# Kernel optimization log

Measured on AMD Instinct MI355X. Metric: run time of the kernel, lower is better.

The kernel has to match this reference:

```python
import jax, jax.numpy as jnp
import numpy as np

D_MODEL = 1024
N_HEADS = 16
HEAD_DIM = 64
T = 4096
ROT = HEAD_DIM // 2          # 32 channels get rotary
PAIR = ROT // 2              # 16 cos/sin frequencies
EPS = 1e-6
SCALE = 0.12                 # constant attention scale (not 1/sqrt(d))
ROPE_BASE = 10000.0
VOCAB = 50257


def setup_inputs() -> dict:
    key = jax.random.key(0)
    k_x, k_qkv, k_o, k_tok = jax.random.split(key, 4)
    bound = 0.5 / np.sqrt(D_MODEL)
    x = jax.random.normal(k_x, (1, T, D_MODEL), dtype=jnp.float32)
    w_qkv = jax.random.uniform(k_qkv, (3 * D_MODEL, D_MODEL), jnp.float32, -bound, bound)
    # module uses zero_init for w_o; use small random so output is non-trivial
    w_o = jax.random.uniform(k_o, (D_MODEL, D_MODEL), jnp.float32, -bound, bound)
    q_norm_w = jnp.ones((HEAD_DIM,), jnp.float32)
    k_norm_w = jnp.ones((HEAD_DIM,), jnp.float32)
    tokens = jax.random.randint(k_tok, (1, T), 0, VOCAB, dtype=jnp.int64)
    pos = jnp.arange(T, dtype=jnp.int64)
    # RotaryCache: inv_freq over pair dims, cos/sin of t * inv_freq
    inv_freq = 1.0 / (ROPE_BASE ** (jnp.arange(PAIR, dtype=jnp.float32) / PAIR))
    freqs = jnp.arange(T, dtype=jnp.float32)[:, None] * inv_freq[None, :]  # [T, PAIR]
    return {
        "x": x, "tokens": tokens, "pos": pos,
        "w_qkv": w_qkv, "w_o": w_o,
        "q_norm_w": q_norm_w, "k_norm_w": k_norm_w,
        "cos": jnp.cos(freqs), "sin": jnp.sin(freqs),
        "window_tokens": 1024, "block_size": 128,
    }


def _rmsnorm(x, w):
    var = jnp.mean(x * x, axis=-1, keepdims=True)
    return x * jax.lax.rsqrt(var + EPS) * w


def reference(x, tokens, pos, w_qkv, w_o, q_norm_w, k_norm_w, cos, sin,
              window_tokens, block_size):
    B, Tq, C = x.shape
    H, Dh = N_HEADS, HEAD_DIM
    qkv = x @ w_qkv.T                                  # [B, T, 3C]
    q, k, v = jnp.split(qkv, 3, axis=-1)

    def to_bhtd(t):
        return t.reshape(B, Tq, H, Dh).transpose(0, 2, 1, 3)
    q, k, v = to_bhtd(q), to_bhtd(k), to_bhtd(v)

    q = _rmsnorm(q, q_norm_w)
    k = _rmsnorm(k, k_norm_w)

    # half-truncated RoPE: rotate first ROT channels pairwise (even/odd)
    c = cos[pos][None, None]                           # [1,1,T,PAIR]
    s = sin[pos][None, None]

    def rope_rotate(t):
        t1, t2 = t[..., :ROT], t[..., ROT:]
        even, odd = t1[..., 0::2], t1[..., 1::2]
        r_even = even * c - odd * s
        r_odd = even * s + odd * c
        t1r = jnp.stack([r_even, r_odd], axis=-1).reshape(t1.shape)
        return jnp.concatenate([t1r, t2], axis=-1)

    q = rope_rotate(q)
    k = rope_rotate(k)

    v = v * 0.5                                        # no value-embed branch

    scores = jnp.einsum('bhtd,bhsd->bhts', q, k) * SCALE
    idx = jnp.arange(Tq)
    diff = idx[:, None] - idx[None, :]
    allowed = (diff >= 0) & (diff < window_tokens)     # sliding causal window
    scores = jnp.where(allowed, scores, -jnp.inf)
    p = jax.nn.softmax(scores, axis=-1)
    out = jnp.einsum('bhts,bhsd->bhtd', p, v)
    out = out.transpose(0, 2, 1, 3).reshape(B, Tq, C)
    return out @ w_o.T
```

## Files before the change

### kernel.cpp

```cpp
#include <hip/hip_runtime.h>


typedef __bf16 bf16x8 __attribute__((ext_vector_type(8)));
typedef __bf16 bf16x2 __attribute__((ext_vector_type(2)));
typedef float f32x4 __attribute__((ext_vector_type(4)));
typedef unsigned short u16x8 __attribute__((ext_vector_type(8)));
typedef unsigned short u16x4 __attribute__((ext_vector_type(4)));

#define MFMA16(a, b, c) __builtin_amdgcn_mfma_f32_16x16x32_bf16((a), (b), (c), 0, 0, 0)

__device__ __forceinline__ unsigned short f2bf(float f) {
    unsigned int u = __float_as_uint(f);
    u += 0x7fffu + ((u >> 16) & 1u);
    return (unsigned short)(u >> 16);
}
__device__ __forceinline__ float bf2f(unsigned short h) {
    return __uint_as_float(((unsigned int)h) << 16);
}
__device__ __forceinline__ unsigned int pk2bf(float a, float b) {
#if __has_builtin(__builtin_amdgcn_cvt_pk_bf16_f32)
    bf16x2 v = __builtin_amdgcn_cvt_pk_bf16_f32(a, b);
    return __builtin_bit_cast(unsigned int, v);
#else
    return (unsigned int)f2bf(a) | ((unsigned int)f2bf(b) << 16);
#endif
}

__device__ __forceinline__ void gl_lds16(const void* g, void* l) {
    typedef __attribute__((address_space(1))) unsigned int GU;
    typedef __attribute__((address_space(3))) unsigned int LU;
    __builtin_amdgcn_global_load_lds((GU*)(unsigned long long)g,
                                     (LU*)(unsigned int)(unsigned long long)l,
                                     16, 0, 0);
}

__global__ void cvt_bf16_kernel(const float* __restrict__ src,
                                unsigned short* __restrict__ dst, int n4) {
    int i = blockIdx.x * blockDim.x + threadIdx.x;
    if (i >= n4) return;
    float4 f = ((const float4*)src)[i];
    u16x4 o;
    o[0] = f2bf(f.x); o[1] = f2bf(f.y); o[2] = f2bf(f.z); o[3] = f2bf(f.w);
    ((u16x4*)dst)[i] = o;
}

template <int BM, bool F32OUT>
__global__ __launch_bounds__(256) void gemm_bt(
    const unsigned short* __restrict__ A,
    const unsigned short* __restrict__ Bt,
    void* __restrict__ Cp, int N, int K) {
    __shared__ unsigned short As[BM * 32];
    __shared__ unsigned short Bs[128 * 32];
    constexpr int MT = BM / 32;
    const int tid = threadIdx.x;
    const int wave = tid >> 6, lane = tid & 63;
    const int quad = lane >> 4, l16 = lane & 15;
    const int m0 = blockIdx.x * BM, n0 = blockIdx.y * 128;
    const int wm = (wave >> 1) * (BM / 2), wn = (wave & 1) * 64;

    f32x4 acc[MT][4];
#pragma unroll
    for (int i = 0; i < MT; ++i)
#pragma unroll
        for (int j = 0; j < 4; ++j) acc[i][j] = (f32x4){0.f, 0.f, 0.f, 0.f};

    for (int k0 = 0; k0 < K; k0 += 32) {
#pragma unroll
        for (int i = 0; i < BM / 64; ++i) {
            const int c = wave * (BM / 64) + i;
            const int e = (c * 64 + lane) * 8;
            const int r = e >> 5, col = e & 31;
            gl_lds16(A + (size_t)(m0 + r) * K + (k0 + col), &As[c * 512]);
        }
#pragma unroll
        for (int i = 0; i < 2; ++i) {
            const int c = wave * 2 + i;
            const int e = (c * 64 + lane) * 8;
            const int r = e >> 5, col = e & 31;
            gl_lds16(Bt + (size_t)(n0 + r) * K + (k0 + col), &Bs[c * 512]);
        }
        __syncthreads();
        bf16x8 af[MT], bfr[4];
#pragma unroll
        for (int mt = 0; mt < MT; ++mt)
            af[mt] = *(const bf16x8*)&As[(wm + mt * 16 + l16) * 32 + quad * 8];
#pragma unroll
        for (int nt = 0; nt < 4; ++nt)
            bfr[nt] = *(const bf16x8*)&Bs[(wn + nt * 16 + l16) * 32 + quad * 8];
#pragma unroll
        for (int mt = 0; mt < MT; ++mt)
#pragma unroll
            for (int nt = 0; nt < 4; ++nt)
                acc[mt][nt] = MFMA16(af[mt], bfr[nt], acc[mt][nt]);
        __syncthreads();
    }
#pragma unroll
    for (int mt = 0; mt < MT; ++mt)
#pragma unroll
        for (int nt = 0; nt < 4; ++nt)
#pragma unroll
            for (int r = 0; r < 4; ++r) {
                const int row = m0 + wm + mt * 16 + quad * 4 + r;
                const int col = n0 + wn + nt * 16 + l16;
                const float v = acc[mt][nt][r];
                if (F32OUT)
                    ((float*)Cp)[(size_t)row * N + col] = v;
                else
                    ((unsigned short*)Cp)[(size_t)row * N + col] = f2bf(v);
            }
}

__global__ __launch_bounds__(256) void rope_pack_kernel(
    const unsigned short* __restrict__ qkv,
    const float* __restrict__ cosb, const float* __restrict__ sinb,
    const float* __restrict__ qw, const float* __restrict__ kw,
    unsigned short* __restrict__ Qb,
    unsigned short* __restrict__ Kb,
    unsigned short* __restrict__ Vt)
{
    __shared__ unsigned short vlds[64][65];
    const int h = blockIdx.y;
    const int t0 = blockIdx.x * 64;
    const int tid = threadIdx.x;
    const int tl = tid >> 2, dq = tid & 3;
    const int t = t0 + tl;
    const unsigned short* base = qkv + (size_t)t * 3072 + h * 64 + dq * 16;

    float q[16], k[16], v[16];
    {
        u16x8 a0 = *(const u16x8*)(base);
        u16x8 a1 = *(const u16x8*)(base + 8);
        u16x8 b0 = *(const u16x8*)(base + 1024);
        u16x8 b1 = *(const u16x8*)(base + 1032);
        u16x8 c0 = *(const u16x8*)(base + 2048);
        u16x8 c1 = *(const u16x8*)(base + 2056);
#pragma unroll
        for (int i = 0; i < 8; ++i) {
            q[i] = bf2f(a0[i]); q[8 + i] = bf2f(a1[i]);
            k[i] = bf2f(b0[i]); k[8 + i] = bf2f(b1[i]);
            v[i] = bf2f(c0[i]); v[8 + i] = bf2f(c1[i]);
        }
    }
    float sq = 0.f, sk = 0.f;
#pragma unroll
    for (int i = 0; i < 16; ++i) { sq += q[i] * q[i]; sk += k[i] * k[i]; }
    sq += __shfl_xor(sq, 1); sq += __shfl_xor(sq, 2);
    sk += __shfl_xor(sk, 1); sk += __shfl_xor(sk, 2);
    const float rq = rsqrtf(sq * (1.f / 64.f) + 1e-6f);
    const float rk = rsqrtf(sk * (1.f / 64.f) + 1e-6f);
#pragma unroll
    for (int i = 0; i < 16; ++i) {
        q[i] *= rq * qw[dq * 16 + i];
        k[i] *= rk * kw[dq * 16 + i];
    }
    if (dq < 2) {
#pragma unroll
        for (int p = 0; p < 8; ++p) {
            const int gp = dq * 8 + p;
            const float c = cosb[t * 16 + gp], s = sinb[t * 16 + gp];
            float e = q[2 * p], o = q[2 * p + 1];
            q[2 * p] = e * c - o * s; q[2 * p + 1] = e * s + o * c;
            e = k[2 * p]; o = k[2 * p + 1];
            k[2 * p] = e * c - o * s; k[2 * p + 1] = e * s + o * c;
        }
    }
    const size_t oo = ((size_t)h * 4096 + t) * 64 + dq * 16;
    u16x8 w0, w1;
#pragma unroll
    for (int i = 0; i < 8; ++i) { w0[i] = f2bf(q[i]); w1[i] = f2bf(q[8 + i]); }
    *(u16x8*)(Qb + oo) = w0; *(u16x8*)(Qb + oo + 8) = w1;
#pragma unroll
    for (int i = 0; i < 8; ++i) { w0[i] = f2bf(k[i]); w1[i] = f2bf(k[8 + i]); }
    *(u16x8*)(Kb + oo) = w0; *(u16x8*)(Kb + oo + 8) = w1;

#pragma unroll
    for (int i = 0; i < 16; ++i) vlds[tl][dq * 16 + i] = f2bf(v[i] * 0.5f);
    __syncthreads();
#pragma unroll
    for (int i = 0; i < 8; ++i) { w0[i] = vlds[dq * 16 + i][tl]; w1[i] = vlds[dq * 16 + 8 + i][tl]; }
    const size_t vo = ((size_t)h * 64 + tl) * 4096 + t0 + dq * 16;
    *(u16x8*)(Vt + vo) = w0; *(u16x8*)(Vt + vo + 8) = w1;
}

#define PSTR 72

template <int MODE>
__device__ __forceinline__ void attn_step(
    int s0, int tq, int wave, int quad, int l16, int krow, int kcol,
    const unsigned short* __restrict__ Kh, const unsigned short* __restrict__ Vh,
    unsigned short* Ks0, unsigned short* Ks1,
    unsigned short* Vs0, unsigned short* Vs1, unsigned short* Pw,
    const bf16x8 qf0, const bf16x8 qf1, f32x4 (&o)[4], float& lsum)
{
    __syncthreads();
    const unsigned short* kb = Kh + (size_t)(s0 + krow) * 64 + kcol;
    const unsigned short* vb = Vh + (size_t)krow * 4096 + s0 + kcol;
    gl_lds16(kb,      &Ks0[wave * 512]);
    gl_lds16(kb + 32, &Ks1[wave * 512]);
    gl_lds16(vb,      &Vs0[wave * 512]);
    gl_lds16(vb + 32, &Vs1[wave * 512]);
    __syncthreads();

    const float c = 0.17312340490667046f;
#pragma unroll
    for (int i = 0; i < 4; ++i) {
        const bf16x8 kf0 = *(const bf16x8*)&Ks0[(i * 16 + l16) * 32 + quad * 8];
        const bf16x8 kf1 = *(const bf16x8*)&Ks1[(i * 16 + l16) * 32 + quad * 8];
        f32x4 z = (f32x4){0.f, 0.f, 0.f, 0.f};
        z = MFMA16(kf0, qf0, z);
        z = MFMA16(kf1, qf1, z);
        float p[4];
#pragma unroll
        for (int r = 0; r < 4; ++r) {
            float e = exp2f(z[r] * c);
            if (MODE == 1) {
                const int s = s0 + i * 16 + quad * 4 + r;
                e = ((tq - s) < 1024) ? e : 0.f;
            }
            if (MODE == 2) {
                const int s = s0 + i * 16 + quad * 4 + r;
                e = (s <= tq) ? e : 0.f;
            }
            p[r] = e;
            lsum += e;
        }
        uint2 pk;
        pk.x = pk2bf(p[0], p[1]);
        pk.y = pk2bf(p[2], p[3]);
        *(uint2*)&Pw[l16 * PSTR + i * 16 + quad * 4] = pk;
    }
    const bf16x8 pf0 = *(const bf16x8*)&Pw[l16 * PSTR + quad * 8];
    const bf16x8 pf1 = *(const bf16x8*)&Pw[l16 * PSTR + 32 + quad * 8];
#pragma unroll
    for (int dt = 0; dt < 4; ++dt) {
        const bf16x8 vf0 = *(const bf16x8*)&Vs0[(dt * 16 + l16) * 32 + quad * 8];
        const bf16x8 vf1 = *(const bf16x8*)&Vs1[(dt * 16 + l16) * 32 + quad * 8];
        o[dt] = MFMA16(pf0, vf0, o[dt]);
        o[dt] = MFMA16(pf1, vf1, o[dt]);
    }
}

__global__ __launch_bounds__(256) void attn_kernel(
    const unsigned short* __restrict__ Qb,
    const unsigned short* __restrict__ Kb,
    const unsigned short* __restrict__ Vt,
    unsigned short* __restrict__ att)
{
    __shared__ unsigned short Ks0[64 * 32];
    __shared__ unsigned short Ks1[64 * 32];
    __shared__ unsigned short Vs0[64 * 32];
    __shared__ unsigned short Vs1[64 * 32];
    __shared__ unsigned short P[4][16 * PSTR];

    const int h = blockIdx.y;
    const int t0 = blockIdx.x * 64;
    const int tid = threadIdx.x;
    const int wave = tid >> 6, lane = tid & 63;
    const int quad = lane >> 4, l16 = lane & 15;
    const int qt0 = t0 + wave * 16;
    const int tq = qt0 + l16;
    const int krow = tid >> 2, kcol = (tid & 3) * 8;

    const unsigned short* Qh = Qb + (size_t)h * 4096 * 64;
    const unsigned short* Kh = Kb + (size_t)h * 4096 * 64;
    const unsigned short* Vh = Vt + (size_t)h * 64 * 4096;

    const bf16x8 qf0 = *(const bf16x8*)&Qh[(qt0 + l16) * 64 + quad * 8];
    const bf16x8 qf1 = *(const bf16x8*)&Qh[(qt0 + l16) * 64 + 32 + quad * 8];

    f32x4 o[4];
#pragma unroll
    for (int dt = 0; dt < 4; ++dt) o[dt] = (f32x4){0.f, 0.f, 0.f, 0.f};
    float lsum = 0.f;
    unsigned short* Pw = P[wave];

    int s0 = (t0 >= 1024) ? (t0 - 1024) : 0;
    if (t0 >= 1024) {
        attn_step<1>(s0, tq, wave, quad, l16, krow, kcol, Kh, Vh,
                     Ks0, Ks1, Vs0, Vs1, Pw, qf0, qf1, o, lsum);
        s0 += 64;
    }
    for (; s0 < t0; s0 += 64)
        attn_step<0>(s0, tq, wave, quad, l16, krow, kcol, Kh, Vh,
                     Ks0, Ks1, Vs0, Vs1, Pw, qf0, qf1, o, lsum);
    attn_step<2>(t0, tq, wave, quad, l16, krow, kcol, Kh, Vh,
                 Ks0, Ks1, Vs0, Vs1, Pw, qf0, qf1, o, lsum);

    lsum += __shfl_xor(lsum, 16);
    lsum += __shfl_xor(lsum, 32);
    float lr[4];
#pragma unroll
    for (int r = 0; r < 4; ++r) lr[r] = 1.f / __shfl(lsum, quad * 4 + r);
#pragma unroll
    for (int dt = 0; dt < 4; ++dt)
#pragma unroll
        for (int r = 0; r < 4; ++r)
            att[(size_t)(qt0 + quad * 4 + r) * 1024 + h * 64 + dt * 16 + l16] =
                f2bf(o[dt][r] * lr[r]);
}

extern "C" void kernel_launch(void* const* d_in, const int* in_sizes, int n_in,
                              void* d_out, int out_size, void* d_ws, size_t ws_size,
                              hipStream_t stream) {
    const float* x    = (const float*)d_in[0];
    const float* wqkv = (const float*)d_in[3];
    const float* wo   = (const float*)d_in[4];
    const float* qw   = (const float*)d_in[5];
    const float* kw   = (const float*)d_in[6];
    const float* cosb = (const float*)d_in[7];
    const float* sinb = (const float*)d_in[8];

    char* ws = (char*)d_ws;
    if (ws_size < (size_t)72 * 1024 * 1024) return;
    unsigned short* xb    = (unsigned short*)(ws + ((size_t)0 << 20));
    unsigned short* wqkvb = (unsigned short*)(ws + ((size_t)8 << 20));
    unsigned short* wob   = (unsigned short*)(ws + ((size_t)14 << 20));
    unsigned short* qkvb  = (unsigned short*)(ws + ((size_t)16 << 20));
    unsigned short* Qb    = (unsigned short*)(ws + ((size_t)40 << 20));
    unsigned short* Kb    = (unsigned short*)(ws + ((size_t)48 << 20));
    unsigned short* Vt    = (unsigned short*)(ws + ((size_t)56 << 20));
    unsigned short* attb  = (unsigned short*)(ws + ((size_t)64 << 20));

    cvt_bf16_kernel<<<4096, 256, 0, stream>>>(x, xb, 4096 * 1024 / 4);
    cvt_bf16_kernel<<<3072, 256, 0, stream>>>(wqkv, wqkvb, 3072 * 1024 / 4);
    cvt_bf16_kernel<<<1024, 256, 0, stream>>>(wo, wob, 1024 * 1024 / 4);

    gemm_bt<128, false><<<dim3(32, 24), 256, 0, stream>>>(xb, wqkvb, qkvb, 3072, 1024);

    rope_pack_kernel<<<dim3(64, 16), 256, 0, stream>>>(qkvb, cosb, sinb, qw, kw, Qb, Kb, Vt);

    attn_kernel<<<dim3(64, 16), 256, 0, stream>>>(Qb, Kb, Vt, attb);

    gemm_bt<64, true><<<dim3(64, 8), 256, 0, stream>>>(attb, wob, (float*)d_out, 1024, 1024);
}
```

Before: 213.9 us.

## Fuse RMSNorm/RoPE/V-transpose into QKV GEMM epilogue and merge conversion kernels

The QKV GEMM epilogue now applies per-head RMSNorm, half RoPE and the V scale-and-transpose straight from the accumulators. This removes the separate rope_pack kernel and the bf16 qkv intermediate round-trip through memory. The three fp32-to-bf16 conversions are merged into one launch. The attention grid is flattened and remapped so adjacent blocks cover different heads. The epilogue writes scalar bf16 values with strided stores, which may coalesce worse than before.

```diff
diff --git a/kernel.cpp b/kernel.cpp
--- a/kernel.cpp
+++ b/kernel.cpp
@@ -34,152 +34,131 @@
                                      16, 0, 0);
 }
 
-__global__ void cvt_bf16_kernel(const float* __restrict__ src,
-                                unsigned short* __restrict__ dst, int n4) {
-    int i = blockIdx.x * blockDim.x + threadIdx.x;
-    if (i >= n4) return;
-    float4 f = ((const float4*)src)[i];
+__global__ void cvt3_kernel(const float* __restrict__ x,
+                            const float* __restrict__ wqkv,
+                            const float* __restrict__ wo,
+                            unsigned short* __restrict__ xb,
+                            unsigned short* __restrict__ wqkvb,
+                            unsigned short* __restrict__ wob) {
+    int i = blockIdx.x * 256 + threadIdx.x;
+    const float* src;
+    unsigned short* dst;
+    int off;
+    if (i < 1048576) { src = x; dst = xb; off = i; }
+    else if (i < 1835008) { src = wqkv; dst = wqkvb; off = i - 1048576; }
+    else { src = wo; dst = wob; off = i - 1835008; }
+    float4 f = ((const float4*)src)[off];
     u16x4 o;
     o[0] = f2bf(f.x); o[1] = f2bf(f.y); o[2] = f2bf(f.z); o[3] = f2bf(f.w);
-    ((u16x4*)dst)[i] = o;
-}
-
-template <int BM, bool F32OUT>
-__global__ __launch_bounds__(256) void gemm_bt(
+    ((u16x4*)dst)[off] = o;
+}
+
+__global__ __launch_bounds__(256) void gemm_qkv(
     const unsigned short* __restrict__ A,
     const unsigned short* __restrict__ Bt,
-    void* __restrict__ Cp, int N, int K) {
-    __shared__ unsigned short As[BM * 32];
-    __shared__ unsigned short Bs[128 * 32];
-    constexpr int MT = BM / 32;
-    const int tid = threadIdx.x;
-    const int wave = tid >> 6, lane = tid & 63;
-    const int quad = lane >> 4, l16 = lane & 15;
-    const int m0 = blockIdx.x * BM, n0 = blockIdx.y * 128;
-    const int wm = (wave >> 1) * (BM / 2), wn = (wave & 1) * 64;
-
-    f32x4 acc[MT][4];
-#pragma unroll
-    for (int i = 0; i < MT; ++i)
-#pragma unroll
-        for (int j = 0; j < 4; ++j) acc[i][j] = (f32x4){0.f, 0.f, 0.f, 0.f};
-
-    for (int k0 = 0; k0 < K; k0 += 32) {
-#pragma unroll
-        for (int i = 0; i < BM / 64; ++i) {
-            const int c = wave * (BM / 64) + i;
-            const int e = (c * 64 + lane) * 8;
-            const int r = e >> 5, col = e & 31;
-            gl_lds16(A + (size_t)(m0 + r) * K + (k0 + col), &As[c * 512]);
-        }
-#pragma unroll
-        for (int i = 0; i < 2; ++i) {
-            const int c = wave * 2 + i;
-            const int e = (c * 64 + lane) * 8;
-            const int r = e >> 5, col = e & 31;
-            gl_lds16(Bt + (size_t)(n0 + r) * K + (k0 + col), &Bs[c * 512]);
-        }
-        __syncthreads();
-        bf16x8 af[MT], bfr[4];
-#pragma unroll
-        for (int mt = 0; mt < MT; ++mt)
-            af[mt] = *(const bf16x8*)&As[(wm + mt * 16 + l16) * 32 + quad * 8];
-#pragma unroll
-        for (int nt = 0; nt < 4; ++nt)
-            bfr[nt] = *(const bf16x8*)&Bs[(wn + nt * 16 + l16) * 32 + quad * 8];
-#pragma unroll
-        for (int mt = 0; mt < MT; ++mt)
-#pragma unroll
-            for (int nt = 0; nt < 4; ++nt)
-                acc[mt][nt] = MFMA16(af[mt], bfr[nt], acc[mt][nt]);
-        __syncthreads();
-    }
-#pragma unroll
-    for (int mt = 0; mt < MT; ++mt)
-#pragma unroll
-        for (int nt = 0; nt < 4; ++nt)
-#pragma unroll
-            for (int r = 0; r < 4; ++r) {
-                const int row = m0 + wm + mt * 16 + quad * 4 + r;
-                const int col = n0 + wn + nt * 16 + l16;
-                const float v = acc[mt][nt][r];
-                if (F32OUT)
-                    ((float*)Cp)[(size_t)row * N + col] = v;
-                else
-                    ((unsigned short*)Cp)[(size_t)row * N + col] = f2bf(v);
-            }
-}
-
-__global__ __launch_bounds__(256) void rope_pack_kernel(
-    const unsigned short* __restrict__ qkv,
     const float* __restrict__ cosb, const float* __restrict__ sinb,
     const float* __restrict__ qw, const float* __restrict__ kw,
     unsigned short* __restrict__ Qb,
     unsigned short* __restrict__ Kb,
     unsigned short* __restrict__ Vt)
 {
-    __shared__ unsigned short vlds[64][65];
-    const int h = blockIdx.y;
-    const int t0 = blockIdx.x * 64;
+    __shared__ unsigned short As[128 * 32];
+    __shared__ unsigned short Bs[128 * 32];
+    __shared__ unsigned short tb[4][64 * 16];
     const int tid = threadIdx.x;
-    const int tl = tid >> 2, dq = tid & 3;
-    const int t = t0 + tl;
-    const unsigned short* base = qkv + (size_t)t * 3072 + h * 64 + dq * 16;
-
-    float q[16], k[16], v[16];
-    {
-        u16x8 a0 = *(const u16x8*)(base);
-        u16x8 a1 = *(const u16x8*)(base + 8);
-        u16x8 b0 = *(const u16x8*)(base + 1024);
-        u16x8 b1 = *(const u16x8*)(base + 1032);
-        u16x8 c0 = *(const u16x8*)(base + 2048);
-        u16x8 c1 = *(const u16x8*)(base + 2056);
-#pragma unroll
-        for (int i = 0; i < 8; ++i) {
-            q[i] = bf2f(a0[i]); q[8 + i] = bf2f(a1[i]);
-            k[i] = bf2f(b0[i]); k[8 + i] = bf2f(b1[i]);
-            v[i] = bf2f(c0[i]); v[8 + i] = bf2f(c1[i]);
-        }
-    }
-    float sq = 0.f, sk = 0.f;
-#pragma unroll
-    for (int i = 0; i < 16; ++i) { sq += q[i] * q[i]; sk += k[i] * k[i]; }
-    sq += __shfl_xor(sq, 1); sq += __shfl_xor(sq, 2);
-    sk += __shfl_xor(sk, 1); sk += __shfl_xor(sk, 2);
-    const float rq = rsqrtf(sq * (1.f / 64.f) + 1e-6f);
-    const float rk = rsqrtf(sk * (1.f / 64.f) + 1e-6f);
-#pragma unroll
-    for (int i = 0; i < 16; ++i) {
-        q[i] *= rq * qw[dq * 16 + i];
-        k[i] *= rk * kw[dq * 16 + i];
-    }
-    if (dq < 2) {
-#pragma unroll
-        for (int p = 0; p < 8; ++p) {
-            const int gp = dq * 8 + p;
-            const float c = cosb[t * 16 + gp], s = sinb[t * 16 + gp];
-            float e = q[2 * p], o = q[2 * p + 1];
-            q[2 * p] = e * c - o * s; q[2 * p + 1] = e * s + o * c;
-            e = k[2 * p]; o = k[2 * p + 1];
-            k[2 * p] = e * c - o * s; k[2 * p + 1] = e * s + o * c;
-        }
-    }
-    const size_t oo = ((size_t)h * 4096 + t) * 64 + dq * 16;
-    u16x8 w0, w1;
-#pragma unroll
-    for (int i = 0; i < 8; ++i) { w0[i] = f2bf(q[i]); w1[i] = f2bf(q[8 + i]); }
-    *(u16x8*)(Qb + oo) = w0; *(u16x8*)(Qb + oo + 8) = w1;
-#pragma unroll
-    for (int i = 0; i < 8; ++i) { w0[i] = f2bf(k[i]); w1[i] = f2bf(k[8 + i]); }
-    *(u16x8*)(Kb + oo) = w0; *(u16x8*)(Kb + oo + 8) = w1;
-
-#pragma unroll
-    for (int i = 0; i < 16; ++i) vlds[tl][dq * 16 + i] = f2bf(v[i] * 0.5f);
-    __syncthreads();
-#pragma unroll
-    for (int i = 0; i < 8; ++i) { w0[i] = vlds[dq * 16 + i][tl]; w1[i] = vlds[dq * 16 + 8 + i][tl]; }
-    const size_t vo = ((size_t)h * 64 + tl) * 4096 + t0 + dq * 16;
-    *(u16x8*)(Vt + vo) = w0; *(u16x8*)(Vt + vo + 8) = w1;
+    const int wave = tid >> 6, lane = tid & 63;
+    const int quad = lane >> 4, l16 = lane & 15;
+    const int m0 = blockIdx.x * 128, n0 = blockIdx.y * 128;
+    const int wm = (wave >> 1) * 64, wn = (wave & 1) * 64;
+    (void)wn;
+
+    f32x4 acc[4][4];
+#pragma unroll
+    for (int i = 0; i < 4; ++i)
+#pragma unroll
+        for (int j = 0; j < 4; ++j) acc[i][j] = (f32x4){0.f, 0.f, 0.f, 0.f};
+
+    for (int k0 = 0; k0 < 1024; k0 += 32) {
+#pragma unroll
+        for (int i = 0; i < 2; ++i) {
+            const int c = wave * 2 + i;
+            const int e = (c * 64 + lane) * 8;
+            const int r = e >> 5, col = e & 31;
+            gl_lds16(A + (size_t)(m0 + r) * 1024 + (k0 + col), &As[c * 512]);
+            gl_lds16(Bt + (size_t)(n0 + r) * 1024 + (k0 + col), &Bs[c * 512]);
+        }
+        __syncthreads();
+        bf16x8 af[4], bfr[4];
+#pragma unroll
+        for (int mt = 0; mt < 4; ++mt)
+            af[mt] = *(const bf16x8*)&As[(wm + mt * 16 + l16) * 32 + quad * 8];
+#pragma unroll
+        for (int nt = 0; nt < 4; ++nt)
+            bfr[nt] = *(const bf16x8*)&Bs[((wave & 1) * 64 + nt * 16 + l16) * 32 + quad * 8];
+#pragma unroll
+        for (int mt = 0; mt < 4; ++mt)
+#pragma unroll
+            for (int nt = 0; nt < 4; ++nt)
+                acc[mt][nt] = MFMA16(af[mt], bfr[nt], acc[mt][nt]);
+        __syncthreads();
+    }
+
+    const int region = blockIdx.y >> 3;
+    const int h = ((blockIdx.y & 7) << 1) + (wave & 1);
+
+    if (region < 2) {
+        const float* wgt = region ? kw : qw;
+        unsigned short* dst = region ? Kb : Qb;
+        float w[4];
+#pragma unroll
+        for (int nt = 0; nt < 4; ++nt) w[nt] = wgt[nt * 16 + l16];
+#pragma unroll
+        for (int mt = 0; mt < 4; ++mt)
+#pragma unroll
+            for (int r = 0; r < 4; ++r) {
+                const int row = m0 + wm + mt * 16 + quad * 4 + r;
+                float ss = 0.f;
+#pragma unroll
+                for (int nt = 0; nt < 4; ++nt)
+                    ss += acc[mt][nt][r] * acc[mt][nt][r];
+                ss += __shfl_xor(ss, 1); ss += __shfl_xor(ss, 2);
+                ss += __shfl_xor(ss, 4); ss += __shfl_xor(ss, 8);
+                const float rn = rsqrtf(ss * (1.f / 64.f) + 1e-6f);
+                float val[4];
+#pragma unroll
+                for (int nt = 0; nt < 4; ++nt)
+                    val[nt] = acc[mt][nt][r] * rn * w[nt];
+#pragma unroll
+                for (int nt = 0; nt < 2; ++nt) {
+                    const float prt = __shfl_xor(val[nt], 1);
+                    const int p = nt * 8 + (l16 >> 1);
+                    const float c = cosb[row * 16 + p];
+                    const float s = sinb[row * 16 + p];
+                    val[nt] = (l16 & 1) ? (prt * s + val[nt] * c)
+                                        : (val[nt] * c - prt * s);
+                }
+                const size_t ob = ((size_t)h * 4096 + row) * 64;
+#pragma unroll
+                for (int nt = 0; nt < 4; ++nt)
+                    dst[ob + nt * 16 + l16] = f2bf(val[nt]);
+            }
+    } else {
+        unsigned short* tbw = tb[wave];
+#pragma unroll
+        for (int mt = 0; mt < 4; ++mt) {
+#pragma unroll
+            for (int nt = 0; nt < 4; ++nt)
+#pragma unroll
+                for (int r = 0; r < 4; ++r)
+                    tbw[(nt * 16 + l16) * 16 + quad * 4 + r] =
+                        f2bf(acc[mt][nt][r] * 0.5f);
+            u16x8 v0 = *(const u16x8*)&tbw[lane * 16];
+            u16x8 v1 = *(const u16x8*)&tbw[lane * 16 + 8];
+            const size_t vo = ((size_t)h * 64 + lane) * 4096 + m0 + wm + mt * 16;
+            *(u16x8*)&Vt[vo] = v0;
+            *(u16x8*)&Vt[vo + 8] = v1;
+        }
+    }
 }
 
 #define PSTR 72
@@ -252,8 +231,10 @@
     __shared__ unsigned short Vs1[64 * 32];
     __shared__ unsigned short P[4][16 * PSTR];
 
-    const int h = blockIdx.y;
-    const int t0 = blockIdx.x * 64;
+    const int bid = blockIdx.x;
+    const int h = ((bid & 7) << 1) | ((bid >> 3) & 1);
+    const int t0 = (bid >> 4) * 64;
+
     const int tid = threadIdx.x;
     const int wave = tid >> 6, lane = tid & 63;
     const int quad = lane >> 4, l16 = lane & 15;
@@ -297,6 +278,72 @@
         for (int r = 0; r < 4; ++r)
             att[(size_t)(qt0 + quad * 4 + r) * 1024 + h * 64 + dt * 16 + l16] =
                 f2bf(o[dt][r] * lr[r]);
+}
+
+template <int BM, bool F32OUT>
+__global__ __launch_bounds__(256) void gemm_bt(
+    const unsigned short* __restrict__ A,
+    const unsigned short* __restrict__ Bt,
+    void* __restrict__ Cp, int N, int K) {
+    __shared__ unsigned short As[BM * 32];
+    __shared__ unsigned short Bs[128 * 32];
+    constexpr int MT = BM / 32;
+    const int tid = threadIdx.x;
+    const int wave = tid >> 6, lane = tid & 63;
+    const int quad = lane >> 4, l16 = lane & 15;
+    const int m0 = blockIdx.x * BM, n0 = blockIdx.y * 128;
+    const int wm = (wave >> 1) * (BM / 2), wn = (wave & 1) * 64;
+
+    f32x4 acc[MT][4];
+#pragma unroll
+    for (int i = 0; i < MT; ++i)
+#pragma unroll
+        for (int j = 0; j < 4; ++j) acc[i][j] = (f32x4){0.f, 0.f, 0.f, 0.f};
+
+    for (int k0 = 0; k0 < K; k0 += 32) {
+#pragma unroll
+        for (int i = 0; i < BM / 64; ++i) {
+            const int c = wave * (BM / 64) + i;
+            const int e = (c * 64 + lane) * 8;
+            const int r = e >> 5, col = e & 31;
+            gl_lds16(A + (size_t)(m0 + r) * K + (k0 + col), &As[c * 512]);
+        }
+#pragma unroll
+        for (int i = 0; i < 2; ++i) {
+            const int c = wave * 2 + i;
+            const int e = (c * 64 + lane) * 8;
+            const int r = e >> 5, col = e & 31;
+            gl_lds16(Bt + (size_t)(n0 + r) * K + (k0 + col), &Bs[c * 512]);
+        }
+        __syncthreads();
+        bf16x8 af[MT], bfr[4];
+#pragma unroll
+        for (int mt = 0; mt < MT; ++mt)
+            af[mt] = *(const bf16x8*)&As[(wm + mt * 16 + l16) * 32 + quad * 8];
+#pragma unroll
+        for (int nt = 0; nt < 4; ++nt)
+            bfr[nt] = *(const bf16x8*)&Bs[(wn + nt * 16 + l16) * 32 + quad * 8];
+#pragma unroll
+        for (int mt = 0; mt < MT; ++mt)
+#pragma unroll
+            for (int nt = 0; nt < 4; ++nt)
+                acc[mt][nt] = MFMA16(af[mt], bfr[nt], acc[mt][nt]);
+        __syncthreads();
+    }
+#pragma unroll
+    for (int mt = 0; mt < MT; ++mt)
+#pragma unroll
+        for (int nt = 0; nt < 4; ++nt)
+#pragma unroll
+            for (int r = 0; r < 4; ++r) {
+                const int row = m0 + wm + mt * 16 + quad * 4 + r;
+                const int col = n0 + wn + nt * 16 + l16;
+                const float v = acc[mt][nt][r];
+                if (F32OUT)
+                    ((float*)Cp)[(size_t)row * N + col] = v;
+                else
+                    ((unsigned short*)Cp)[(size_t)row * N + col] = f2bf(v);
+            }
 }
 
 extern "C" void kernel_launch(void* const* d_in, const int* in_sizes, int n_in,
@@ -311,25 +358,21 @@
     const float* sinb = (const float*)d_in[8];
 
     char* ws = (char*)d_ws;
-    if (ws_size < (size_t)72 * 1024 * 1024) return;
+    if (ws_size < (size_t)48 * 1024 * 1024) return;
     unsigned short* xb    = (unsigned short*)(ws + ((size_t)0 << 20));
     unsigned short* wqkvb = (unsigned short*)(ws + ((size_t)8 << 20));
     unsigned short* wob   = (unsigned short*)(ws + ((size_t)14 << 20));
-    unsigned short* qkvb  = (unsigned short*)(ws + ((size_t)16 << 20));
-    unsigned short* Qb    = (unsigned short*)(ws + ((size_t)40 << 20));
-    unsigned short* Kb    = (unsigned short*)(ws + ((size_t)48 << 20));
-    unsigned short* Vt    = (unsigned short*)(ws + ((size_t)56 << 20));
-    unsigned short* attb  = (unsigned short*)(ws + ((size_t)64 << 20));
-
-    cvt_bf16_kernel<<<4096, 256, 0, stream>>>(x, xb, 4096 * 1024 / 4);
-    cvt_bf16_kernel<<<3072, 256, 0, stream>>>(wqkv, wqkvb, 3072 * 1024 / 4);
-    cvt_bf16_kernel<<<1024, 256, 0, stream>>>(wo, wob, 1024 * 1024 / 4);
-
-    gemm_bt<128, false><<<dim3(32, 24), 256, 0, stream>>>(xb, wqkvb, qkvb, 3072, 1024);
-
-    rope_pack_kernel<<<dim3(64, 16), 256, 0, stream>>>(qkvb, cosb, sinb, qw, kw, Qb, Kb, Vt);
-
-    attn_kernel<<<dim3(64, 16), 256, 0, stream>>>(Qb, Kb, Vt, attb);
+    unsigned short* Qb    = (unsigned short*)(ws + ((size_t)16 << 20));
+    unsigned short* Kb    = (unsigned short*)(ws + ((size_t)24 << 20));
+    unsigned short* Vt    = (unsigned short*)(ws + ((size_t)32 << 20));
+    unsigned short* attb  = (unsigned short*)(ws + ((size_t)40 << 20));
+
+    cvt3_kernel<<<8192, 256, 0, stream>>>(x, wqkv, wo, xb, wqkvb, wob);
+
+    gemm_qkv<<<dim3(32, 24), 256, 0, stream>>>(xb, wqkvb, cosb, sinb, qw, kw,
+                                               Qb, Kb, Vt);
+
+    attn_kernel<<<1024, 256, 0, stream>>>(Qb, Kb, Vt, attb);
 
     gemm_bt<64, true><<<dim3(64, 8), 256, 0, stream>>>(attb, wob, (float*)d_out, 1024, 1024);
 }
```

Measured after the change: 209.0 us. -2.3%, faster.
